# Optimization experiments

Measured on AMD Instinct MI355X. Metric: run time of the kernel, lower is better.

The kernel has to match this reference:

```python
import jax, jax.numpy as jnp
import numpy as np

CONF_THRES = 0.6   # non_max_suppression default
IOU_THRES = 0.45   # non_max_suppression default
MAX_WH = 4096.0    # class-offset trick constant
MAX_DET = 300
NC = 80


def xywh2xyxy(b):
    xy, wh = b[:, :2], b[:, 2:4]
    return jnp.concatenate([xy - wh / 2, xy + wh / 2], axis=1)


def box_iou(a, b):
    # a: [N,4], b: [M,4] xyxy -> [N,M]
    area_a = (a[:, 2] - a[:, 0]) * (a[:, 3] - a[:, 1])
    area_b = (b[:, 2] - b[:, 0]) * (b[:, 3] - b[:, 1])
    lt = jnp.maximum(a[:, None, :2], b[None, :, :2])
    rb = jnp.minimum(a[:, None, 2:], b[None, :, 2:])
    wh = jnp.clip(rb - lt, 0.0)
    inter = wh[..., 0] * wh[..., 1]
    return inter / (area_a[:, None] + area_b[None, :] - inter + 1e-9)


def nms_image(x):
    # x: [N, 85] = [xywh, obj, 80 class logits]
    N = x.shape[0]
    logits = x[:, 5:]
    obj = x[:, 4]
    cls = logits * obj[:, None]          # x[:,5:] *= x[:,4:5]
    box = xywh2xyxy(x[:, :4])
    conf = cls.max(axis=1)
    j = jnp.argmax(cls, axis=1)
    valid = (obj > CONF_THRES) & (conf > CONF_THRES)
    scores = jnp.where(valid, conf, -1.0)  # invalid sort last, never suppress
    boxes_off = box + (j.astype(x.dtype) * MAX_WH)[:, None]  # class offset NMS

    order = jnp.argsort(-scores)
    iou = box_iou(boxes_off[order], boxes_off[order])  # [N,N]
    idxs = jnp.arange(N)

    def body(i, keep):
        sup = (iou[i] > IOU_THRES) & (idxs > i) & keep[i]
        return keep & ~sup

    keep = jax.lax.fori_loop(0, N, body, valid[order])

    # rows = [xyxy, conf, cls_idx, 80 logits] in score-sorted order
    rows = jnp.concatenate([
        box[order],
        conf[order][:, None],
        j[order].astype(x.dtype)[:, None],
        logits[order],
    ], axis=1)  # [N, 86]

    rank = jnp.cumsum(keep) - 1
    dest = jnp.where(keep & (rank < MAX_DET), rank, MAX_DET)  # dropped -> slot MAX_DET
    out = jnp.zeros((MAX_DET + 1, rows.shape[1]), x.dtype).at[dest].set(rows)
    return out[:MAX_DET]  # [300, 86]; zero rows = no detection


def setup_inputs() -> dict:
    key = jax.random.key(0)
    score = jax.random.normal(key, (32, 425, 17, 17), dtype=jnp.float32)
    return {"score": score}


def reference(score):
    B, C, H, W = score.shape
    # view(B, 425, H*W).transpose(1,2).view(B, H*W*5, 85)
    pred = score.reshape(B, C, H * W)
    pred = jnp.transpose(pred, (0, 2, 1)).reshape(B, H * W * 5, 85)
    return jax.vmap(nms_image)(pred)  # [B, 300, 86] = [xyxy, conf, cls, 80 logits]
```

## Files before the change

kernel.cpp:

```cpp
#include <hip/hip_runtime.h>

#define NPRED 1445
#define RAWSTR 1472
#define NCLS  80
#define MAXDET 300
#define OUTC  86
#define CONF_T 0.6f
#define IOU_T  0.45f
#define MAX_WH 4096.0f
#define HWSZ  289
#define NIMG  32
#define SLOTS 768
#define MCAP  512
#define EPB   256
#define EWALK 2048

#define OFF_CNT  128
#define OFF_KEYR 256
#define OFF_BOXR 377088
#define OFF_KEY  1130752
#define OFF_SBOX 1327360
#define OFF_ECNT 1720576
#define OFF_EDG  1721600
#define OFF_DST  1983744
#define WS_NEED  2022144

__device__ __forceinline__ unsigned long long bcast64(unsigned long long v, int srcLane) {
    unsigned lo = (unsigned)__builtin_amdgcn_readlane((int)(unsigned)(v & 0xFFFFFFFFULL), srcLane);
    unsigned hi = (unsigned)__builtin_amdgcn_readlane((int)(unsigned)(v >> 32), srcLane);
    return ((unsigned long long)hi << 32) | lo;
}

__global__ __launch_bounds__(128)
void prep_kernel(const float* __restrict__ score, unsigned long long* __restrict__ wsKeyRaw,
                 float4* __restrict__ wsBoxRaw) {
    const int b = blockIdx.x;
    const int ci = blockIdx.y * 128 + threadIdx.x;
    if (ci >= NPRED) return;
    const int t5 = ci / HWSZ;
    const int hw = ci - t5 * HWSZ;
    const int n = hw * 5 + t5;
    const float* base = score + (size_t)b * 425 * HWSZ + (size_t)(t5 * 85) * HWSZ + hw;
    float x = base[0];
    float y = base[HWSZ];
    float w = base[2 * HWSZ];
    float h = base[3 * HWSZ];
    float obj = base[4 * HWSZ];

    float best = -INFINITY; int bj = 0;
    #pragma unroll 16
    for (int k = 0; k < NCLS; ++k) {
        float v = base[(5 + k) * HWSZ] * obj;
        if (v > best) { best = v; bj = k; }
    }

    float wh2 = w * 0.5f, hh2 = h * 0.5f;
    float x1 = x - wh2, y1 = y - hh2, x2 = x + wh2, y2 = y + hh2;
    float off = (float)bj * MAX_WH;

    unsigned long long key = ~0ULL;
    if ((obj > CONF_T) && (best > CONF_T)) {
        unsigned int u = __float_as_uint(best);
        unsigned int desc = ~(u | 0x80000000u);
        key = ((unsigned long long)desc << 32)
            | ((unsigned long long)(unsigned)n << 16)
            | ((unsigned long long)(unsigned)bj << 8);
    }
    wsKeyRaw[b * RAWSTR + ci] = key;
    wsBoxRaw[b * RAWSTR + ci] = make_float4(x1 + off, y1 + off, x2 + off, y2 + off);
}

__global__ __launch_bounds__(1024)
void sort_kernel(const unsigned long long* __restrict__ wsKeyRaw,
                 const float4* __restrict__ wsBoxRaw,
                 int* __restrict__ wsCnt, unsigned long long* __restrict__ wsKey,
                 float4* __restrict__ wsSBox) {
    __shared__ unsigned long long keys[NPRED];
    __shared__ unsigned long long ckeys[SLOTS];
    __shared__ unsigned short cidx[SLOTS];
    __shared__ int wtot[16];
    __shared__ int mTot;
    const int b = blockIdx.x, tid = threadIdx.x;
    const int lane = tid & 63, wid = tid >> 6;

    for (int i = tid; i < NPRED; i += 1024) keys[i] = wsKeyRaw[b * RAWSTR + i];
    __syncthreads();

    const int i0 = tid, i1 = tid + 1024;
    const bool v0 = (keys[i0] >> 63) == 0ULL;
    const bool v1 = (i1 < NPRED) && ((keys[i1] >> 63) == 0ULL);
    int cnt = (int)v0 + (int)v1;
    int inc = cnt;
    #pragma unroll
    for (int m = 1; m < 64; m <<= 1) {
        int v = __shfl_up(inc, m, 64);
        if (lane >= m) inc += v;
    }
    if (lane == 63) wtot[wid] = inc;
    __syncthreads();
    int basep = 0;
    for (int w = 0; w < wid; ++w) basep += wtot[w];
    int pos = basep + inc - cnt;
    if (v0 && pos < SLOTS) cidx[pos] = (unsigned short)i0;
    if (v1 && pos + (int)v0 < SLOTS) cidx[pos + (int)v0] = (unsigned short)i1;
    if (tid == 0) {
        int t = 0;
        for (int w = 0; w < 16; ++w) t += wtot[w];
        mTot = t;
    }
    __syncthreads();
    int M = mTot; if (M > SLOTS) M = SLOTS;
    if (tid == 0) wsCnt[b] = M;
    if (tid < M) ckeys[tid] = keys[cidx[tid]];
    __syncthreads();
    if (tid < M) {
        unsigned long long ki = ckeys[tid];
        int rank = 0;
        #pragma unroll 4
        for (int j = 0; j < M; ++j) rank += (ckeys[j] < ki) ? 1 : 0;
        wsKey[b * SLOTS + rank] = ki;
        wsSBox[b * SLOTS + rank] = wsBoxRaw[b * RAWSTR + cidx[tid]];
    }
}

__global__ __launch_bounds__(512)
void edge_kernel(const int* __restrict__ wsCnt, const float4* __restrict__ wsSBox,
                 int* __restrict__ wsECnt, unsigned int* __restrict__ wsEdges) {
    __shared__ float4 box[MCAP];
    __shared__ int ecnt;
    const int b = blockIdx.x, w = blockIdx.y, tid = threadIdx.x;
    int M = wsCnt[b]; if (M > SLOTS) M = SLOTS;
    if (M > MCAP) { if (tid == 0) wsECnt[b * 8 + w] = 0x7FFFFFFF; return; }
    if (tid == 0) ecnt = 0;
    for (int r = tid; r < M; r += 512) box[r] = wsSBox[b * SLOTS + r];
    __syncthreads();
    const int lane = tid & 63, wid = tid >> 6;
    const int j = (w << 6) + lane;
    float4 jb = make_float4(0.f, 0.f, 0.f, 0.f); float ab = 0.f;
    const bool jok = (j < M);
    if (jok) { jb = box[j]; ab = (jb.z - jb.x) * (jb.w - jb.y); }
    unsigned int* reg = wsEdges + (size_t)(b * 8 + w) * EPB;
    for (int i = wid; i < M; i += 8) {
        float4 cur = box[i];
        float aa = (cur.z - cur.x) * (cur.w - cur.y);
        bool sup = false;
        if (jok && j > i) {
            float ltx = fmaxf(cur.x, jb.x), lty = fmaxf(cur.y, jb.y);
            float rbx = fminf(cur.z, jb.z), rby = fminf(cur.w, jb.w);
            float ww = fmaxf(rbx - ltx, 0.0f), hh = fmaxf(rby - lty, 0.0f);
            float inter = ww * hh;
            float denom = ((aa + ab) - inter) + 1e-9f;
            sup = (inter / denom) > IOU_T;
        }
        unsigned long long mask = __ballot(sup);
        if (lane == 0 && mask) {
            int pc = __popcll(mask);
            int eb = atomicAdd(&ecnt, pc);
            int k = 0;
            while (mask) {
                int bit = __ffsll((long long)mask) - 1;
                mask &= mask - 1;
                int p = eb + k;
                if (p < EPB) reg[p] = ((unsigned)i << 9) | (unsigned)((w << 6) + bit);
                ++k;
            }
        }
    }
    __syncthreads();
    if (tid == 0) wsECnt[b * 8 + w] = ecnt;
}

struct ScanSh {
    union {
        struct {
            float x1[SLOTS], y1[SLOTS], x2[SLOTS], y2[SLOTS];
            unsigned char kp[SLOTS];
        } fb;
        struct { unsigned int eraw[EWALK]; unsigned int esrt[EWALK]; } e;
    } u;
    int ec[8];
    int eoff[9];
    int over;
};

__global__ __launch_bounds__(256)
void scan_kernel(const int* __restrict__ wsCnt, const int* __restrict__ wsECnt,
                 const unsigned int* __restrict__ wsEdges, const float4* __restrict__ wsSBox,
                 int* __restrict__ wsKept, int* __restrict__ wsDst) {
    __shared__ ScanSh sh;
    const int b = blockIdx.x, tid = threadIdx.x, lane = tid & 63;
    int M = wsCnt[b]; if (M > SLOTS) M = SLOTS;
    if (tid < 8) sh.ec[tid] = wsECnt[b * 8 + tid];
    if (tid == 0) sh.over = 0;
    __syncthreads();
    if (tid == 0) {
        int o = 0;
        for (int w = 0; w < 8; ++w) {
            sh.eoff[w] = o;
            int c = sh.ec[w];
            if (c > EPB) { sh.over = 1; c = EPB; }
            o += c;
        }
        sh.eoff[8] = o;
    }
    __syncthreads();
    const bool fast = (M <= MCAP) && (sh.over == 0);
    const int Etot = sh.eoff[8];

    if (fast) {
        for (int w = 0; w < 8; ++w) {
            int c = sh.ec[w]; if (c > EPB) c = EPB;
            const unsigned int* reg = wsEdges + (size_t)(b * 8 + w) * EPB;
            for (int e2 = tid; e2 < c; e2 += 256) sh.u.e.eraw[sh.eoff[w] + e2] = reg[e2];
        }
        __syncthreads();
        for (int e2 = tid; e2 < Etot; e2 += 256) {
            unsigned int ke = sh.u.e.eraw[e2];
            int rank = 0;
            for (int j2 = 0; j2 < Etot; ++j2) rank += (sh.u.e.eraw[j2] < ke) ? 1 : 0;
            sh.u.e.esrt[rank] = ke;
        }
        __syncthreads();
        if (tid >= 64) return;
        unsigned long long Kw = 0ULL;
        { int rem = M - (lane << 6);
          if (rem >= 64) Kw = ~0ULL; else if (rem > 0) Kw = (~0ULL) >> (64 - rem); }
        unsigned int A[8], B[8];
#define LOADE(buf, bs) { _Pragma("unroll") for (int k = 0; k < 8; ++k) { \
        int e2 = (bs) + k; buf[k] = (e2 < Etot) ? sh.u.e.esrt[e2] : 0xFFFFFFFFu; } }
#define PROCE(buf) { _Pragma("unroll") for (int k = 0; k < 8; ++k) { \
        unsigned int ek = buf[k]; \
        if (ek != 0xFFFFFFFFu) { \
            int ei = (int)(ek >> 9), ej = (int)(ek & 511u); \
            unsigned long long kwi = bcast64(Kw, ei >> 6); \
            if ((kwi >> (ei & 63)) & 1ULL) { \
                if (lane == (ej >> 6)) Kw &= ~(1ULL << (ej & 63)); \
            } } } }
        LOADE(A, 0)
        for (int e = 0; e < Etot; e += 16) {
            LOADE(B, e + 8)
            PROCE(A)
            LOADE(A, e + 16)
            PROCE(B)
        }
#undef LOADE
#undef PROCE
        int myc = __popcll(Kw);
        int incc = myc;
        #pragma unroll
        for (int m = 1; m < 64; m <<= 1) {
            int v = __shfl_up(incc, m, 64);
            if (lane >= m) incc += v;
        }
        int tot = __shfl(incc, 63, 64);
        if (lane == 0) wsKept[b] = (tot < MAXDET) ? tot : MAXDET;
        int r = incc - myc;
        unsigned long long kw = Kw;
        while (kw) {
            int i = __ffsll((long long)kw) - 1;
            kw &= kw - 1;
            if (r < MAXDET) wsDst[b * MAXDET + r] = (lane << 6) + i;
            ++r;
        }
    } else {
        for (int r = tid; r < M; r += 256) {
            float4 v = wsSBox[b * SLOTS + r];
            sh.u.fb.x1[r] = v.x; sh.u.fb.y1[r] = v.y;
            sh.u.fb.x2[r] = v.z; sh.u.fb.y2[r] = v.w; sh.u.fb.kp[r] = 1;
        }
        __syncthreads();
        for (int i = 0; i < M; ++i) {
            if (sh.u.fb.kp[i]) {
                float ax1 = sh.u.fb.x1[i], ay1 = sh.u.fb.y1[i];
                float ax2 = sh.u.fb.x2[i], ay2 = sh.u.fb.y2[i];
                float aa = (ax2 - ax1) * (ay2 - ay1);
                for (int r = i + 1 + tid; r < M; r += 256) {
                    float bx1 = sh.u.fb.x1[r], by1 = sh.u.fb.y1[r];
                    float bx2 = sh.u.fb.x2[r], by2 = sh.u.fb.y2[r];
                    float ab = (bx2 - bx1) * (by2 - by1);
                    float ltx = fmaxf(ax1, bx1), lty = fmaxf(ay1, by1);
                    float rbx = fminf(ax2, bx2), rby = fminf(ay2, by2);
                    float ww = fmaxf(rbx - ltx, 0.0f), hh = fmaxf(rby - lty, 0.0f);
                    float inter = ww * hh;
                    float denom = ((aa + ab) - inter) + 1e-9f;
                    if ((inter / denom) > IOU_T) sh.u.fb.kp[r] = 0;
                }
            }
            __syncthreads();
        }
        if (tid == 0) {
            int c2 = 0;
            for (int r = 0; r < M && c2 < MAXDET; ++r)
                if (sh.u.fb.kp[r]) wsDst[b * MAXDET + c2++] = r;
            wsKept[b] = c2;
        }
    }
}

__global__ __launch_bounds__(256)
void out_kernel(const float* __restrict__ score, const int* __restrict__ wsKept,
                const unsigned long long* __restrict__ wsKey,
                const int* __restrict__ wsDst, float* __restrict__ out) {
    const int b = blockIdx.x;
    const int e = blockIdx.y * 256 + threadIdx.x;
    if (e >= MAXDET * OUTC) return;
    const int row = e / OUTC, c = e - row * OUTC;
    float v = 0.0f;
    if (row < wsKept[b]) {
        unsigned long long key = wsKey[b * SLOTS + wsDst[b * MAXDET + row]];
        int n = (int)((key >> 16) & 0xFFFFULL);
        int cls = (int)((key >> 8) & 0xFFULL);
        int hw = n / 5, t5 = n - hw * 5;
        const float* base = score + (size_t)b * 425 * HWSZ + (size_t)(t5 * 85) * HWSZ + hw;
        if (c < 4) {
            float x = base[0];
            float y = base[HWSZ];
            float w = base[2 * HWSZ];
            float h = base[3 * HWSZ];
            float wh2 = w * 0.5f, hh2 = h * 0.5f;
            v = (c == 0) ? (x - wh2) : (c == 1) ? (y - hh2)
              : (c == 2) ? (x + wh2) : (y + hh2);
        } else if (c == 4) {
            v = __uint_as_float((~(unsigned int)(key >> 32)) & 0x7FFFFFFFu);
        } else if (c == 5) {
            v = (float)cls;
        } else {
            v = base[(c - 1) * HWSZ];
        }
    }
    out[(size_t)b * MAXDET * OUTC + e] = v;
}

struct SMemFB {
    float bx1[NPRED], by1[NPRED], bx2[NPRED], by2[NPRED], area[NPRED];
    unsigned short sortedN[NPRED];
    union {
        unsigned long long vkey[NPRED];
        struct { float confR[MAXDET]; unsigned char jclsR[MAXDET]; } oi;
        unsigned char keepFB[NPRED];
    } u;
    unsigned short dstN[MAXDET];
    int validCount;
    int keptCount;
};

__device__ __forceinline__ void conf_argmax(const float* __restrict__ base, float obj,
                                            float& conf, int& bj) {
    float best = -INFINITY; int bjj = 0;
    #pragma unroll 8
    for (int k = 0; k < NCLS; ++k) {
        float v = base[(5 + k) * HWSZ] * obj;
        if (v > best) { best = v; bjj = k; }
    }
    conf = best; bj = bjj;
}

__global__ __launch_bounds__(1024)
void yolo_nms_single(const float* __restrict__ score, float* __restrict__ out) {
    __shared__ SMemFB s;
    const int b = blockIdx.x;
    const int tid = threadIdx.x;
    const float* sb = score + (size_t)b * 425 * HWSZ;
    if (tid == 0) s.validCount = 0;
    __syncthreads();
    for (int ci = tid; ci < NPRED; ci += 1024) {
        int t5 = ci / HWSZ;
        int hw = ci - t5 * HWSZ;
        int n = hw * 5 + t5;
        const float* base = sb + (size_t)(t5 * 85) * HWSZ + hw;
        float x = base[0], y = base[HWSZ], w = base[2 * HWSZ], h = base[3 * HWSZ];
        float obj = base[4 * HWSZ];
        float conf; int bj;
        conf_argmax(base, obj, conf, bj);
        bool valid = (obj > CONF_T) && (conf > CONF_T);
        float wh2 = w * 0.5f, hh2 = h * 0.5f;
        float x1 = x - wh2, y1 = y - hh2, x2 = x + wh2, y2 = y + hh2;
        float off = (float)bj * MAX_WH;
        float ox1 = x1 + off, oy1 = y1 + off, ox2 = x2 + off, oy2 = y2 + off;
        s.bx1[n] = ox1; s.by1[n] = oy1; s.bx2[n] = ox2; s.by2[n] = oy2;
        s.area[n] = (ox2 - ox1) * (oy2 - oy1);
        if (valid) {
            int slot = atomicAdd(&s.validCount, 1);
            unsigned int uu = __float_as_uint(conf);
            unsigned int desc = ~(uu | 0x80000000u);
            s.u.vkey[slot] = ((unsigned long long)desc << 32) | (unsigned int)n;
        }
    }
    __syncthreads();
    const int M = s.validCount;
    for (int vi = tid; vi < M; vi += 1024) {
        unsigned long long ki = s.u.vkey[vi];
        int rank = 0;
        for (int j = 0; j < M; ++j) rank += (s.u.vkey[j] < ki) ? 1 : 0;
        s.sortedN[rank] = (unsigned short)(ki & 0xFFFFULL);
    }
    __syncthreads();
    for (int r = tid; r < M; r += 1024) s.u.keepFB[r] = 1;
    __syncthreads();
    for (int i = 0; i < M; ++i) {
        if (s.u.keepFB[i]) {
            int ni = s.sortedN[i];
            float ax1 = s.bx1[ni], ay1 = s.by1[ni], ax2 = s.bx2[ni], ay2 = s.by2[ni];
            float aa = s.area[ni];
            for (int r = i + 1 + tid; r < M; r += 1024) {
                int nj = s.sortedN[r];
                float ltx = fmaxf(ax1, s.bx1[nj]);
                float lty = fmaxf(ay1, s.by1[nj]);
                float rbx = fminf(ax2, s.bx2[nj]);
                float rby = fminf(ay2, s.by2[nj]);
                float ww = fmaxf(rbx - ltx, 0.0f);
                float hh = fmaxf(rby - lty, 0.0f);
                float inter = ww * hh;
                float denom = ((aa + s.area[nj]) - inter) + 1e-9f;
                if ((inter / denom) > IOU_T) s.u.keepFB[r] = 0;
            }
        }
        __syncthreads();
    }
    if (tid == 0) {
        int cnt = 0;
        for (int r = 0; r < M && cnt < MAXDET; ++r)
            if (s.u.keepFB[r]) s.dstN[cnt++] = s.sortedN[r];
        s.keptCount = cnt;
    }
    __syncthreads();
    const int cnt = s.keptCount;
    if (tid < cnt) {
        int n = s.dstN[tid];
        int hw = n / 5, t5 = n - hw * 5;
        const float* base = sb + (size_t)(t5 * 85) * HWSZ + hw;
        float obj = base[4 * HWSZ];
        float conf; int bj;
        conf_argmax(base, obj, conf, bj);
        s.u.oi.confR[tid] = conf;
        s.u.oi.jclsR[tid] = (unsigned char)bj;
    }
    __syncthreads();
    float* ob = out + (size_t)b * MAXDET * OUTC;
    for (int e = tid; e < MAXDET * OUTC; e += 1024) {
        int row = e / OUTC, c = e - row * OUTC;
        float v = 0.0f;
        if (row < cnt) {
            int n = s.dstN[row];
            int hw = n / 5, t5 = n - hw * 5;
            const float* base = sb + (size_t)(t5 * 85) * HWSZ + hw;
            if (c < 4) {
                float x = base[0], y = base[HWSZ], w = base[2 * HWSZ], h = base[3 * HWSZ];
                float wh2 = w * 0.5f, hh2 = h * 0.5f;
                v = (c == 0) ? (x - wh2) : (c == 1) ? (y - hh2)
                  : (c == 2) ? (x + wh2) : (y + hh2);
            } else if (c == 4) {
                v = s.u.oi.confR[row];
            } else if (c == 5) {
                v = (float)s.u.oi.jclsR[row];
            } else {
                v = base[(c - 1) * HWSZ];
            }
        }
        ob[e] = v;
    }
}

extern "C" void kernel_launch(void* const* d_in, const int* in_sizes, int n_in,
                              void* d_out, int out_size, void* d_ws, size_t ws_size,
                              hipStream_t stream) {
    const float* score = (const float*)d_in[0];
    float* out = (float*)d_out;
    char* ws = (char*)d_ws;
    int* wsKept = (int*)ws;
    int* wsCnt  = (int*)(ws + OFF_CNT);
    unsigned long long* wsKeyRaw = (unsigned long long*)(ws + OFF_KEYR);
    float4* wsBoxRaw = (float4*)(ws + OFF_BOXR);
    unsigned long long* wsKey = (unsigned long long*)(ws + OFF_KEY);
    float4* wsSBox = (float4*)(ws + OFF_SBOX);
    int* wsECnt = (int*)(ws + OFF_ECNT);
    unsigned int* wsEdges = (unsigned int*)(ws + OFF_EDG);
    int* wsDst = (int*)(ws + OFF_DST);

    if (ws_size >= (size_t)WS_NEED) {
        prep_kernel<<<dim3(NIMG, 12), 128, 0, stream>>>(score, wsKeyRaw, wsBoxRaw);
        sort_kernel<<<NIMG, 1024, 0, stream>>>(wsKeyRaw, wsBoxRaw, wsCnt, wsKey, wsSBox);
        edge_kernel<<<dim3(NIMG, 8), 512, 0, stream>>>(wsCnt, wsSBox, wsECnt, wsEdges);
        scan_kernel<<<NIMG, 256, 0, stream>>>(wsCnt, wsECnt, wsEdges, wsSBox, wsKept, wsDst);
        out_kernel<<<dim3(NIMG, 101), 256, 0, stream>>>(score, wsKept, wsKey, wsDst, out);
    } else {
        yolo_nms_single<<<NIMG, 1024, 0, stream>>>(score, out);
    }
}
```

Baseline: 45.85 us.

## Fuse sort, edge and scan kernels into one per-image NMS kernel

Merges the sort, IoU-edge and greedy-scan kernels into a single 1024-thread block per image. Sorted boxes and suppression edges stay in shared memory instead of going through global workspace, which removes two launches and their global round trips. The edge buffer grows to a single shared list, and overflow now falls back to the serial path. The trade-off is that edge computation uses only 32 blocks (one per image) instead of 256, so there is less parallelism across the GPU.

```diff
diff --git a/kernel.cpp b/kernel.cpp
--- a/kernel.cpp
+++ b/kernel.cpp
@@ -12,18 +12,13 @@
 #define NIMG  32
 #define SLOTS 768
 #define MCAP  512
-#define EPB   256
-#define EWALK 2048
-
-#define OFF_CNT  128
+#define EWALK 4096
+
 #define OFF_KEYR 256
 #define OFF_BOXR 377088
 #define OFF_KEY  1130752
-#define OFF_SBOX 1327360
-#define OFF_ECNT 1720576
-#define OFF_EDG  1721600
-#define OFF_DST  1983744
-#define WS_NEED  2022144
+#define OFF_DST  1327360
+#define WS_NEED  1365760
 
 __device__ __forceinline__ unsigned long long bcast64(unsigned long long v, int srcLane) {
     unsigned lo = (unsigned)__builtin_amdgcn_readlane((int)(unsigned)(v & 0xFFFFFFFFULL), srcLane);
@@ -70,25 +65,35 @@
     wsBoxRaw[b * RAWSTR + ci] = make_float4(x1 + off, y1 + off, x2 + off, y2 + off);
 }
 
+struct FusedSh {
+    unsigned long long keys[NPRED];
+    float sx1[SLOTS], sy1[SLOTS], sx2[SLOTS], sy2[SLOTS];
+    union {
+        unsigned long long cke[SLOTS];
+        struct { unsigned int eraw[EWALK]; unsigned int esrt[EWALK]; } e;
+        unsigned char kp[SLOTS];
+    } u;
+    unsigned short cidx[SLOTS];
+    int wtot[16];
+    int mTot, ecnt;
+};
+
 __global__ __launch_bounds__(1024)
-void sort_kernel(const unsigned long long* __restrict__ wsKeyRaw,
-                 const float4* __restrict__ wsBoxRaw,
-                 int* __restrict__ wsCnt, unsigned long long* __restrict__ wsKey,
-                 float4* __restrict__ wsSBox) {
-    __shared__ unsigned long long keys[NPRED];
-    __shared__ unsigned long long ckeys[SLOTS];
-    __shared__ unsigned short cidx[SLOTS];
-    __shared__ int wtot[16];
-    __shared__ int mTot;
+void fused_nms_kernel(const unsigned long long* __restrict__ wsKeyRaw,
+                      const float4* __restrict__ wsBoxRaw,
+                      unsigned long long* __restrict__ wsKey,
+                      int* __restrict__ wsKept, int* __restrict__ wsDst) {
+    __shared__ FusedSh s;
     const int b = blockIdx.x, tid = threadIdx.x;
     const int lane = tid & 63, wid = tid >> 6;
 
-    for (int i = tid; i < NPRED; i += 1024) keys[i] = wsKeyRaw[b * RAWSTR + i];
+    for (int i = tid; i < NPRED; i += 1024) s.keys[i] = wsKeyRaw[b * RAWSTR + i];
+    if (tid == 0) s.ecnt = 0;
     __syncthreads();
 
     const int i0 = tid, i1 = tid + 1024;
-    const bool v0 = (keys[i0] >> 63) == 0ULL;
-    const bool v1 = (i1 < NPRED) && ((keys[i1] >> 63) == 0ULL);
+    const bool v0 = (s.keys[i0] >> 63) == 0ULL;
+    const bool v1 = (i1 < NPRED) && ((s.keys[i1] >> 63) == 0ULL);
     int cnt = (int)v0 + (int)v1;
     int inc = cnt;
     #pragma unroll
@@ -96,129 +101,81 @@
         int v = __shfl_up(inc, m, 64);
         if (lane >= m) inc += v;
     }
-    if (lane == 63) wtot[wid] = inc;
+    if (lane == 63) s.wtot[wid] = inc;
     __syncthreads();
     int basep = 0;
-    for (int w = 0; w < wid; ++w) basep += wtot[w];
+    for (int w = 0; w < wid; ++w) basep += s.wtot[w];
     int pos = basep + inc - cnt;
-    if (v0 && pos < SLOTS) cidx[pos] = (unsigned short)i0;
-    if (v1 && pos + (int)v0 < SLOTS) cidx[pos + (int)v0] = (unsigned short)i1;
+    if (v0 && pos < SLOTS) s.cidx[pos] = (unsigned short)i0;
+    if (v1 && pos + (int)v0 < SLOTS) s.cidx[pos + (int)v0] = (unsigned short)i1;
     if (tid == 0) {
         int t = 0;
-        for (int w = 0; w < 16; ++w) t += wtot[w];
-        mTot = t;
-    }
-    __syncthreads();
-    int M = mTot; if (M > SLOTS) M = SLOTS;
-    if (tid == 0) wsCnt[b] = M;
-    if (tid < M) ckeys[tid] = keys[cidx[tid]];
-    __syncthreads();
+        for (int w = 0; w < 16; ++w) t += s.wtot[w];
+        s.mTot = t;
+    }
+    __syncthreads();
+    int M = s.mTot; if (M > SLOTS) M = SLOTS;
+    if (tid < M) s.u.cke[tid] = s.keys[s.cidx[tid]];
+    __syncthreads();
+
     if (tid < M) {
-        unsigned long long ki = ckeys[tid];
+        unsigned long long ki = s.u.cke[tid];
         int rank = 0;
         #pragma unroll 4
-        for (int j = 0; j < M; ++j) rank += (ckeys[j] < ki) ? 1 : 0;
+        for (int j = 0; j < M; ++j) rank += (s.u.cke[j] < ki) ? 1 : 0;
         wsKey[b * SLOTS + rank] = ki;
-        wsSBox[b * SLOTS + rank] = wsBoxRaw[b * RAWSTR + cidx[tid]];
-    }
-}
-
-__global__ __launch_bounds__(512)
-void edge_kernel(const int* __restrict__ wsCnt, const float4* __restrict__ wsSBox,
-                 int* __restrict__ wsECnt, unsigned int* __restrict__ wsEdges) {
-    __shared__ float4 box[MCAP];
-    __shared__ int ecnt;
-    const int b = blockIdx.x, w = blockIdx.y, tid = threadIdx.x;
-    int M = wsCnt[b]; if (M > SLOTS) M = SLOTS;
-    if (M > MCAP) { if (tid == 0) wsECnt[b * 8 + w] = 0x7FFFFFFF; return; }
-    if (tid == 0) ecnt = 0;
-    for (int r = tid; r < M; r += 512) box[r] = wsSBox[b * SLOTS + r];
-    __syncthreads();
-    const int lane = tid & 63, wid = tid >> 6;
-    const int j = (w << 6) + lane;
-    float4 jb = make_float4(0.f, 0.f, 0.f, 0.f); float ab = 0.f;
-    const bool jok = (j < M);
-    if (jok) { jb = box[j]; ab = (jb.z - jb.x) * (jb.w - jb.y); }
-    unsigned int* reg = wsEdges + (size_t)(b * 8 + w) * EPB;
-    for (int i = wid; i < M; i += 8) {
-        float4 cur = box[i];
-        float aa = (cur.z - cur.x) * (cur.w - cur.y);
-        bool sup = false;
-        if (jok && j > i) {
-            float ltx = fmaxf(cur.x, jb.x), lty = fmaxf(cur.y, jb.y);
-            float rbx = fminf(cur.z, jb.z), rby = fminf(cur.w, jb.w);
-            float ww = fmaxf(rbx - ltx, 0.0f), hh = fmaxf(rby - lty, 0.0f);
-            float inter = ww * hh;
-            float denom = ((aa + ab) - inter) + 1e-9f;
-            sup = (inter / denom) > IOU_T;
-        }
-        unsigned long long mask = __ballot(sup);
-        if (lane == 0 && mask) {
-            int pc = __popcll(mask);
-            int eb = atomicAdd(&ecnt, pc);
-            int k = 0;
-            while (mask) {
-                int bit = __ffsll((long long)mask) - 1;
-                mask &= mask - 1;
-                int p = eb + k;
-                if (p < EPB) reg[p] = ((unsigned)i << 9) | (unsigned)((w << 6) + bit);
-                ++k;
+        float4 bx = wsBoxRaw[b * RAWSTR + s.cidx[tid]];
+        s.sx1[rank] = bx.x; s.sy1[rank] = bx.y; s.sx2[rank] = bx.z; s.sy2[rank] = bx.w;
+    }
+    __syncthreads();
+
+    bool fallback = (M > MCAP);
+    int Etot = 0;
+    if (!fallback) {
+        const int NW = (M + 63) >> 6;
+        for (int i = wid; i < M; i += 16) {
+            float ax1 = s.sx1[i], ay1 = s.sy1[i], ax2 = s.sx2[i], ay2 = s.sy2[i];
+            float aa = (ax2 - ax1) * (ay2 - ay1);
+            for (int w = (i >> 6); w < NW; ++w) {
+                int j = (w << 6) + lane;
+                bool sup = false;
+                if (j < M && j > i) {
+                    float bx1 = s.sx1[j], by1 = s.sy1[j], bx2 = s.sx2[j], by2 = s.sy2[j];
+                    float ab = (bx2 - bx1) * (by2 - by1);
+                    float ltx = fmaxf(ax1, bx1), lty = fmaxf(ay1, by1);
+                    float rbx = fminf(ax2, bx2), rby = fminf(ay2, by2);
+                    float ww = fmaxf(rbx - ltx, 0.0f), hh = fmaxf(rby - lty, 0.0f);
+                    float inter = ww * hh;
+                    float denom = ((aa + ab) - inter) + 1e-9f;
+                    sup = (inter / denom) > IOU_T;
+                }
+                unsigned long long mask = __ballot(sup);
+                if (lane == 0 && mask) {
+                    int pc = __popcll(mask);
+                    int eb = atomicAdd(&s.ecnt, pc);
+                    int k = 0;
+                    while (mask) {
+                        int bit = __ffsll((long long)mask) - 1;
+                        mask &= mask - 1;
+                        int p = eb + k;
+                        if (p < EWALK)
+                            s.u.e.eraw[p] = ((unsigned)i << 9) | (unsigned)((w << 6) + bit);
+                        ++k;
+                    }
+                }
             }
         }
-    }
-    __syncthreads();
-    if (tid == 0) wsECnt[b * 8 + w] = ecnt;
-}
-
-struct ScanSh {
-    union {
-        struct {
-            float x1[SLOTS], y1[SLOTS], x2[SLOTS], y2[SLOTS];
-            unsigned char kp[SLOTS];
-        } fb;
-        struct { unsigned int eraw[EWALK]; unsigned int esrt[EWALK]; } e;
-    } u;
-    int ec[8];
-    int eoff[9];
-    int over;
-};
-
-__global__ __launch_bounds__(256)
-void scan_kernel(const int* __restrict__ wsCnt, const int* __restrict__ wsECnt,
-                 const unsigned int* __restrict__ wsEdges, const float4* __restrict__ wsSBox,
-                 int* __restrict__ wsKept, int* __restrict__ wsDst) {
-    __shared__ ScanSh sh;
-    const int b = blockIdx.x, tid = threadIdx.x, lane = tid & 63;
-    int M = wsCnt[b]; if (M > SLOTS) M = SLOTS;
-    if (tid < 8) sh.ec[tid] = wsECnt[b * 8 + tid];
-    if (tid == 0) sh.over = 0;
-    __syncthreads();
-    if (tid == 0) {
-        int o = 0;
-        for (int w = 0; w < 8; ++w) {
-            sh.eoff[w] = o;
-            int c = sh.ec[w];
-            if (c > EPB) { sh.over = 1; c = EPB; }
-            o += c;
-        }
-        sh.eoff[8] = o;
-    }
-    __syncthreads();
-    const bool fast = (M <= MCAP) && (sh.over == 0);
-    const int Etot = sh.eoff[8];
-
-    if (fast) {
-        for (int w = 0; w < 8; ++w) {
-            int c = sh.ec[w]; if (c > EPB) c = EPB;
-            const unsigned int* reg = wsEdges + (size_t)(b * 8 + w) * EPB;
-            for (int e2 = tid; e2 < c; e2 += 256) sh.u.e.eraw[sh.eoff[w] + e2] = reg[e2];
-        }
         __syncthreads();
-        for (int e2 = tid; e2 < Etot; e2 += 256) {
-            unsigned int ke = sh.u.e.eraw[e2];
+        Etot = s.ecnt;
+        if (Etot > EWALK) fallback = true;
+    }
+
+    if (!fallback) {
+        for (int e2 = tid; e2 < Etot; e2 += 1024) {
+            unsigned int ke = s.u.e.eraw[e2];
             int rank = 0;
-            for (int j2 = 0; j2 < Etot; ++j2) rank += (sh.u.e.eraw[j2] < ke) ? 1 : 0;
-            sh.u.e.esrt[rank] = ke;
+            for (int j2 = 0; j2 < Etot; ++j2) rank += (s.u.e.eraw[j2] < ke) ? 1 : 0;
+            s.u.e.esrt[rank] = ke;
         }
         __syncthreads();
         if (tid >= 64) return;
@@ -227,7 +184,7 @@
           if (rem >= 64) Kw = ~0ULL; else if (rem > 0) Kw = (~0ULL) >> (64 - rem); }
         unsigned int A[8], B[8];
 #define LOADE(buf, bs) { _Pragma("unroll") for (int k = 0; k < 8; ++k) { \
-        int e2 = (bs) + k; buf[k] = (e2 < Etot) ? sh.u.e.esrt[e2] : 0xFFFFFFFFu; } }
+        int e2 = (bs) + k; buf[k] = (e2 < Etot) ? s.u.e.esrt[e2] : 0xFFFFFFFFu; } }
 #define PROCE(buf) { _Pragma("unroll") for (int k = 0; k < 8; ++k) { \
         unsigned int ek = buf[k]; \
         if (ek != 0xFFFFFFFFu) { \
@@ -263,27 +220,22 @@
             ++r;
         }
     } else {
-        for (int r = tid; r < M; r += 256) {
-            float4 v = wsSBox[b * SLOTS + r];
-            sh.u.fb.x1[r] = v.x; sh.u.fb.y1[r] = v.y;
-            sh.u.fb.x2[r] = v.z; sh.u.fb.y2[r] = v.w; sh.u.fb.kp[r] = 1;
-        }
+        __syncthreads();
+        for (int r = tid; r < M; r += 1024) s.u.kp[r] = 1;
         __syncthreads();
         for (int i = 0; i < M; ++i) {
-            if (sh.u.fb.kp[i]) {
-                float ax1 = sh.u.fb.x1[i], ay1 = sh.u.fb.y1[i];
-                float ax2 = sh.u.fb.x2[i], ay2 = sh.u.fb.y2[i];
+            if (s.u.kp[i]) {
+                float ax1 = s.sx1[i], ay1 = s.sy1[i], ax2 = s.sx2[i], ay2 = s.sy2[i];
                 float aa = (ax2 - ax1) * (ay2 - ay1);
-                for (int r = i + 1 + tid; r < M; r += 256) {
-                    float bx1 = sh.u.fb.x1[r], by1 = sh.u.fb.y1[r];
-                    float bx2 = sh.u.fb.x2[r], by2 = sh.u.fb.y2[r];
+                for (int r = i + 1 + tid; r < M; r += 1024) {
+                    float bx1 = s.sx1[r], by1 = s.sy1[r], bx2 = s.sx2[r], by2 = s.sy2[r];
                     float ab = (bx2 - bx1) * (by2 - by1);
                     float ltx = fmaxf(ax1, bx1), lty = fmaxf(ay1, by1);
                     float rbx = fminf(ax2, bx2), rby = fminf(ay2, by2);
                     float ww = fmaxf(rbx - ltx, 0.0f), hh = fmaxf(rby - lty, 0.0f);
                     float inter = ww * hh;
                     float denom = ((aa + ab) - inter) + 1e-9f;
-                    if ((inter / denom) > IOU_T) sh.u.fb.kp[r] = 0;
+                    if ((inter / denom) > IOU_T) s.u.kp[r] = 0;
                 }
             }
             __syncthreads();
@@ -291,7 +243,7 @@
         if (tid == 0) {
             int c2 = 0;
             for (int r = 0; r < M && c2 < MAXDET; ++r)
-                if (sh.u.fb.kp[r]) wsDst[b * MAXDET + c2++] = r;
+                if (s.u.kp[r]) wsDst[b * MAXDET + c2++] = r;
             wsKept[b] = c2;
         }
     }
@@ -468,20 +420,14 @@
     float* out = (float*)d_out;
     char* ws = (char*)d_ws;
     int* wsKept = (int*)ws;
-    int* wsCnt  = (int*)(ws + OFF_CNT);
     unsigned long long* wsKeyRaw = (unsigned long long*)(ws + OFF_KEYR);
     float4* wsBoxRaw = (float4*)(ws + OFF_BOXR);
     unsigned long long* wsKey = (unsigned long long*)(ws + OFF_KEY);
-    float4* wsSBox = (float4*)(ws + OFF_SBOX);
-    int* wsECnt = (int*)(ws + OFF_ECNT);
-    unsigned int* wsEdges = (unsigned int*)(ws + OFF_EDG);
     int* wsDst = (int*)(ws + OFF_DST);
 
     if (ws_size >= (size_t)WS_NEED) {
         prep_kernel<<<dim3(NIMG, 12), 128, 0, stream>>>(score, wsKeyRaw, wsBoxRaw);
-        sort_kernel<<<NIMG, 1024, 0, stream>>>(wsKeyRaw, wsBoxRaw, wsCnt, wsKey, wsSBox);
-        edge_kernel<<<dim3(NIMG, 8), 512, 0, stream>>>(wsCnt, wsSBox, wsECnt, wsEdges);
-        scan_kernel<<<NIMG, 256, 0, stream>>>(wsCnt, wsECnt, wsEdges, wsSBox, wsKept, wsDst);
+        fused_nms_kernel<<<NIMG, 1024, 0, stream>>>(wsKeyRaw, wsBoxRaw, wsKey, wsKept, wsDst);
         out_kernel<<<dim3(NIMG, 101), 256, 0, stream>>>(score, wsKept, wsKey, wsDst, out);
     } else {
         yolo_nms_single<<<NIMG, 1024, 0, stream>>>(score, out);
```

Measured after the change: 66.26 us. 44.5% more time.

## Fuse sort into edge kernel with redundant per-block sorting and triangular i range

Applied to the files above, without the earlier changes.

Merges the sort and edge-building kernels into one launch. Each of the 8 column blocks per image redoes the compaction and rank sort into shared SoA arrays, and only block 0 writes the sorted keys and boxes to global memory. The edge loop now stops at the block's upper column bound (triangular, since j > i) and uses 16 waves. This removes one launch and a global round trip, at the cost of sorting 8 times per image.

```diff
diff --git a/kernel.cpp b/kernel.cpp
--- a/kernel.cpp
+++ b/kernel.cpp
@@ -70,25 +70,32 @@
     wsBoxRaw[b * RAWSTR + ci] = make_float4(x1 + off, y1 + off, x2 + off, y2 + off);
 }
 
+struct EdgeSh {
+    unsigned long long keys[NPRED];
+    unsigned long long cke[SLOTS];
+    unsigned short cidx[SLOTS];
+    float sx1[SLOTS], sy1[SLOTS], sx2[SLOTS], sy2[SLOTS];
+    int wtot[16];
+    int mTot, ecnt;
+};
+
 __global__ __launch_bounds__(1024)
-void sort_kernel(const unsigned long long* __restrict__ wsKeyRaw,
+void edge_kernel(const unsigned long long* __restrict__ wsKeyRaw,
                  const float4* __restrict__ wsBoxRaw,
                  int* __restrict__ wsCnt, unsigned long long* __restrict__ wsKey,
-                 float4* __restrict__ wsSBox) {
-    __shared__ unsigned long long keys[NPRED];
-    __shared__ unsigned long long ckeys[SLOTS];
-    __shared__ unsigned short cidx[SLOTS];
-    __shared__ int wtot[16];
-    __shared__ int mTot;
-    const int b = blockIdx.x, tid = threadIdx.x;
+                 float4* __restrict__ wsSBox,
+                 int* __restrict__ wsECnt, unsigned int* __restrict__ wsEdges) {
+    __shared__ EdgeSh s;
+    const int b = blockIdx.x, w = blockIdx.y, tid = threadIdx.x;
     const int lane = tid & 63, wid = tid >> 6;
 
-    for (int i = tid; i < NPRED; i += 1024) keys[i] = wsKeyRaw[b * RAWSTR + i];
+    for (int i = tid; i < NPRED; i += 1024) s.keys[i] = wsKeyRaw[b * RAWSTR + i];
+    if (tid == 0) s.ecnt = 0;
     __syncthreads();
 
     const int i0 = tid, i1 = tid + 1024;
-    const bool v0 = (keys[i0] >> 63) == 0ULL;
-    const bool v1 = (i1 < NPRED) && ((keys[i1] >> 63) == 0ULL);
+    const bool v0 = (s.keys[i0] >> 63) == 0ULL;
+    const bool v1 = (i1 < NPRED) && ((s.keys[i1] >> 63) == 0ULL);
     int cnt = (int)v0 + (int)v1;
     int inc = cnt;
     #pragma unroll
@@ -96,57 +103,56 @@
         int v = __shfl_up(inc, m, 64);
         if (lane >= m) inc += v;
     }
-    if (lane == 63) wtot[wid] = inc;
+    if (lane == 63) s.wtot[wid] = inc;
     __syncthreads();
     int basep = 0;
-    for (int w = 0; w < wid; ++w) basep += wtot[w];
+    for (int w2 = 0; w2 < wid; ++w2) basep += s.wtot[w2];
     int pos = basep + inc - cnt;
-    if (v0 && pos < SLOTS) cidx[pos] = (unsigned short)i0;
-    if (v1 && pos + (int)v0 < SLOTS) cidx[pos + (int)v0] = (unsigned short)i1;
+    if (v0 && pos < SLOTS) s.cidx[pos] = (unsigned short)i0;
+    if (v1 && pos + (int)v0 < SLOTS) s.cidx[pos + (int)v0] = (unsigned short)i1;
     if (tid == 0) {
         int t = 0;
-        for (int w = 0; w < 16; ++w) t += wtot[w];
-        mTot = t;
-    }
-    __syncthreads();
-    int M = mTot; if (M > SLOTS) M = SLOTS;
-    if (tid == 0) wsCnt[b] = M;
-    if (tid < M) ckeys[tid] = keys[cidx[tid]];
-    __syncthreads();
+        for (int w2 = 0; w2 < 16; ++w2) t += s.wtot[w2];
+        s.mTot = t;
+    }
+    __syncthreads();
+    int M = s.mTot; if (M > SLOTS) M = SLOTS;
+    if (tid < M) s.cke[tid] = s.keys[s.cidx[tid]];
+    __syncthreads();
+
     if (tid < M) {
-        unsigned long long ki = ckeys[tid];
+        unsigned long long ki = s.cke[tid];
         int rank = 0;
         #pragma unroll 4
-        for (int j = 0; j < M; ++j) rank += (ckeys[j] < ki) ? 1 : 0;
-        wsKey[b * SLOTS + rank] = ki;
-        wsSBox[b * SLOTS + rank] = wsBoxRaw[b * RAWSTR + cidx[tid]];
-    }
-}
-
-__global__ __launch_bounds__(512)
-void edge_kernel(const int* __restrict__ wsCnt, const float4* __restrict__ wsSBox,
-                 int* __restrict__ wsECnt, unsigned int* __restrict__ wsEdges) {
-    __shared__ float4 box[MCAP];
-    __shared__ int ecnt;
-    const int b = blockIdx.x, w = blockIdx.y, tid = threadIdx.x;
-    int M = wsCnt[b]; if (M > SLOTS) M = SLOTS;
+        for (int j2 = 0; j2 < M; ++j2) rank += (s.cke[j2] < ki) ? 1 : 0;
+        float4 bx = wsBoxRaw[b * RAWSTR + s.cidx[tid]];
+        s.sx1[rank] = bx.x; s.sy1[rank] = bx.y; s.sx2[rank] = bx.z; s.sy2[rank] = bx.w;
+        if (w == 0) {
+            wsKey[b * SLOTS + rank] = ki;
+            wsSBox[b * SLOTS + rank] = bx;
+        }
+    }
+    if (w == 0 && tid == 0) wsCnt[b] = M;
+    __syncthreads();
+
     if (M > MCAP) { if (tid == 0) wsECnt[b * 8 + w] = 0x7FFFFFFF; return; }
-    if (tid == 0) ecnt = 0;
-    for (int r = tid; r < M; r += 512) box[r] = wsSBox[b * SLOTS + r];
-    __syncthreads();
-    const int lane = tid & 63, wid = tid >> 6;
+
+    unsigned int* reg = wsEdges + (size_t)(b * 8 + w) * EPB;
     const int j = (w << 6) + lane;
-    float4 jb = make_float4(0.f, 0.f, 0.f, 0.f); float ab = 0.f;
+    float jx1 = 0.f, jy1 = 0.f, jx2 = 0.f, jy2 = 0.f, ab = 0.f;
     const bool jok = (j < M);
-    if (jok) { jb = box[j]; ab = (jb.z - jb.x) * (jb.w - jb.y); }
-    unsigned int* reg = wsEdges + (size_t)(b * 8 + w) * EPB;
-    for (int i = wid; i < M; i += 8) {
-        float4 cur = box[i];
-        float aa = (cur.z - cur.x) * (cur.w - cur.y);
+    if (jok) {
+        jx1 = s.sx1[j]; jy1 = s.sy1[j]; jx2 = s.sx2[j]; jy2 = s.sy2[j];
+        ab = (jx2 - jx1) * (jy2 - jy1);
+    }
+    int ilim = (w + 1) << 6; if (ilim > M) ilim = M;
+    for (int i = wid; i < ilim; i += 16) {
+        float ax1 = s.sx1[i], ay1 = s.sy1[i], ax2 = s.sx2[i], ay2 = s.sy2[i];
+        float aa = (ax2 - ax1) * (ay2 - ay1);
         bool sup = false;
         if (jok && j > i) {
-            float ltx = fmaxf(cur.x, jb.x), lty = fmaxf(cur.y, jb.y);
-            float rbx = fminf(cur.z, jb.z), rby = fminf(cur.w, jb.w);
+            float ltx = fmaxf(ax1, jx1), lty = fmaxf(ay1, jy1);
+            float rbx = fminf(ax2, jx2), rby = fminf(ay2, jy2);
             float ww = fmaxf(rbx - ltx, 0.0f), hh = fmaxf(rby - lty, 0.0f);
             float inter = ww * hh;
             float denom = ((aa + ab) - inter) + 1e-9f;
@@ -155,7 +161,7 @@
         unsigned long long mask = __ballot(sup);
         if (lane == 0 && mask) {
             int pc = __popcll(mask);
-            int eb = atomicAdd(&ecnt, pc);
+            int eb = atomicAdd(&s.ecnt, pc);
             int k = 0;
             while (mask) {
                 int bit = __ffsll((long long)mask) - 1;
@@ -167,7 +173,7 @@
         }
     }
     __syncthreads();
-    if (tid == 0) wsECnt[b * 8 + w] = ecnt;
+    if (tid == 0) wsECnt[b * 8 + w] = s.ecnt;
 }
 
 struct ScanSh {
@@ -479,8 +485,8 @@
 
     if (ws_size >= (size_t)WS_NEED) {
         prep_kernel<<<dim3(NIMG, 12), 128, 0, stream>>>(score, wsKeyRaw, wsBoxRaw);
-        sort_kernel<<<NIMG, 1024, 0, stream>>>(wsKeyRaw, wsBoxRaw, wsCnt, wsKey, wsSBox);
-        edge_kernel<<<dim3(NIMG, 8), 512, 0, stream>>>(wsCnt, wsSBox, wsECnt, wsEdges);
+        edge_kernel<<<dim3(NIMG, 8), 1024, 0, stream>>>(wsKeyRaw, wsBoxRaw, wsCnt,
+                                                        wsKey, wsSBox, wsECnt, wsEdges);
         scan_kernel<<<NIMG, 256, 0, stream>>>(wsCnt, wsECnt, wsEdges, wsSBox, wsKept, wsDst);
         out_kernel<<<dim3(NIMG, 101), 256, 0, stream>>>(score, wsKept, wsKey, wsDst, out);
     } else {
```

After: 42.69 us (median of 3 runs). -6.9%, faster.
